# Performance work log

Measured on AMD Instinct MI355X. Metric: run time of the kernel, lower is better.

The kernel has to match this reference:

```python
import jax, jax.numpy as jnp
import numpy as np

EPS = 1e-5

def setup_inputs() -> dict:
    key = jax.random.key(0)
    ks = jax.random.split(key, 8)
    b, c, p, h = 8, 128, 2048, 4
    inp = {
        "input": jax.random.normal(ks[0], (b, c, p), jnp.float32),
        "gamma": jnp.ones((c,), jnp.float32),
        "beta": jnp.zeros((c,), jnp.float32),
        "Wq": jax.random.normal(ks[1], (c * h, c), jnp.float32) * (c ** -0.5),
        "bq": jnp.zeros((c * h,), jnp.float32),
        "Wk": jax.random.normal(ks[2], (c * h, c), jnp.float32) * (c ** -0.5),
        "bk": jnp.zeros((c * h,), jnp.float32),
        "Wv": jax.random.normal(ks[3], (c * h, c), jnp.float32) * (c ** -0.5),
        "bv": jnp.zeros((c * h,), jnp.float32),
        "Wo": jax.random.normal(ks[4], (c, c * h), jnp.float32) * ((c * h) ** -0.5),
        "bo": jnp.zeros((c,), jnp.float32),
    }
    return inp


def reference(input, gamma, beta, Wq, bq, Wk, bk, Wv, bv, Wo, bo):
    b, c, p = input.shape
    h = Wq.shape[0] // c
    # BatchNorm1d (training-mode batch stats): mean/var per channel over (batch, points)
    mean = jnp.mean(input, axis=(0, 2), keepdims=True)          # [1,c,1]
    var = jnp.mean((input - mean) ** 2, axis=(0, 2), keepdims=True)
    x = (input - mean) * jax.lax.rsqrt(var + EPS)
    x = x * gamma[None, :, None] + beta[None, :, None]
    # 1x1 conv projections == channel matmuls; then split c*h -> (c, h)
    q = (jnp.einsum('oc,bcp->bop', Wq, x) + bq[None, :, None]).reshape(b, c, h, p)
    k = (jnp.einsum('oc,bcp->bop', Wk, x) + bk[None, :, None]).reshape(b, c, h, p)
    v = (jnp.einsum('oc,bcp->bop', Wv, x) + bv[None, :, None]).reshape(b, c, h, p)
    # attention over points; scale by c**-0.5
    weight = jnp.einsum('bchi,bchj->bhij', q, k) * (c ** -0.5)   # [b,h,p,p]
    weight = jax.nn.softmax(weight, axis=3)
    att = jnp.einsum('bhij,bchj->bchi', weight, v)               # [b,c,h,p]
    att = att.reshape(b, c * h, p)
    out = jnp.einsum('oc,bcp->bop', Wo, att) + bo[None, :, None]
    return out + input
```

## Files before the change

kernel.cpp:

```cpp
#include <hip/hip_runtime.h>
#include <hip/hip_bf16.h>

#define NB 8
#define NC 128
#define NP 2048
#define NH 4
#define NCH 512

typedef __attribute__((ext_vector_type(8))) short bf16x8;
typedef __attribute__((ext_vector_type(16))) float f32x16;

__device__ __forceinline__ float bf2f(unsigned short u) {
  return __uint_as_float(((unsigned)u) << 16);
}
__device__ __forceinline__ unsigned short f2bf(float f) {
  __hip_bfloat16 h = __float2bfloat16(f);
  return *reinterpret_cast<unsigned short*>(&h);
}
__device__ __forceinline__ unsigned pk2(float lo, float hi) {
  return (unsigned)f2bf(lo) | ((unsigned)f2bf(hi) << 16);
}
__device__ __forceinline__ void gload_lds16(const void* g, void* l) {
  __builtin_amdgcn_global_load_lds(
      (const __attribute__((address_space(1))) void*)g,
      (__attribute__((address_space(3))) void*)l, 16, 0, 0);
}
__device__ __forceinline__ void plswap(unsigned& a, unsigned& b) {
  asm volatile("v_permlane32_swap_b32 %0, %1" : "+v"(a), "+v"(b));
}

__global__ __launch_bounds__(256) void bn_partial(
    const float* __restrict__ in, float* __restrict__ psum,
    float* __restrict__ psum2) {
  int c = blockIdx.x >> 2, qtr = blockIdx.x & 3;
  int t = threadIdx.x;
  float s = 0.f, s2 = 0.f;
  for (int b = 0; b < NB; ++b) {
    const float* ptr = in + ((size_t)b * NC + c) * NP + qtr * 512;
    #pragma unroll
    for (int p = 0; p < 2; ++p) {
      float v = ptr[p * 256 + t];
      s += v; s2 += v * v;
    }
  }
  for (int off = 32; off; off >>= 1) {
    s += __shfl_down(s, off, 64);
    s2 += __shfl_down(s2, off, 64);
  }
  __shared__ float red[8];
  int lane = t & 63, wid = t >> 6;
  if (!lane) { red[wid] = s; red[wid + 4] = s2; }
  __syncthreads();
  if (!t) {
    psum[blockIdx.x] = red[0] + red[1] + red[2] + red[3];
    psum2[blockIdx.x] = red[4] + red[5] + red[6] + red[7];
  }
}

__global__ __launch_bounds__(512, 2) void qkv_proj(
    const float* __restrict__ in, const float* __restrict__ gamma,
    const float* __restrict__ beta, const float* __restrict__ psum,
    const float* __restrict__ psum2, const float* __restrict__ Wq,
    const float* __restrict__ bq, const float* __restrict__ Wk,
    const float* __restrict__ bk, const float* __restrict__ Wv,
    const float* __restrict__ bv, unsigned short* __restrict__ qws,
    unsigned short* __restrict__ kws, unsigned short* __restrict__ vws) {
  __shared__ float sc[128], sh[128], bias[1536];
  __shared__ __align__(16) unsigned short Xt[64][136];
  int t = threadIdx.x;
  int pt = blockIdx.x & 31, b = blockIdx.x >> 5;
  int p0 = pt * 64;
  if (t < 128) {
    float s = psum[t * 4] + psum[t * 4 + 1] + psum[t * 4 + 2] + psum[t * 4 + 3];
    float s2 = psum2[t * 4] + psum2[t * 4 + 1] + psum2[t * 4 + 2] + psum2[t * 4 + 3];
    const float invn = 1.f / (NB * NP);
    float mean = s * invn, var = s2 * invn - mean * mean;
    float scl = gamma[t] * rsqrtf(var + 1e-5f);
    sc[t] = scl; sh[t] = beta[t] - mean * scl;
  }
  bias[t] = bq[t]; bias[512 + t] = bk[t]; bias[1024 + t] = bv[t];
  __syncthreads();
  {
    int p = t & 63, c0 = (t >> 6) * 16;
    const float* src = in + ((size_t)b * NC + c0) * NP + p0 + p;
    #pragma unroll
    for (int cc = 0; cc < 16; ++cc) {
      float v = src[(size_t)cc * NP];
      Xt[p][c0 + cc] = f2bf(v * sc[c0 + cc] + sh[c0 + cc]);
    }
  }
  __syncthreads();
  int w = t >> 6, lane = t & 63, l31 = lane & 31, h5 = lane >> 5;
  #pragma unroll 1
  for (int s = 0; s < 3; ++s) {
    int strip = s * 8 + w;
    int proj = strip >> 3, within = (strip & 7) * 64;
    const float* W = proj == 0 ? Wq : (proj == 1 ? Wk : Wv);
    f32x16 acc[2][2] = {};
    #pragma unroll
    for (int ks = 0; ks < 8; ++ks) {
      bf16x8 af[2], bf[2];
      #pragma unroll
      for (int mt = 0; mt < 2; ++mt) {
        const float* wr = W + (size_t)(within + mt * 32 + l31) * NC + ks * 16 + h5 * 8;
        float4 a = *(const float4*)wr, b4 = *(const float4*)(wr + 4);
        union { bf16x8 v; unsigned u[4]; } uu;
        uu.u[0] = pk2(a.x, a.y); uu.u[1] = pk2(a.z, a.w);
        uu.u[2] = pk2(b4.x, b4.y); uu.u[3] = pk2(b4.z, b4.w);
        af[mt] = uu.v;
      }
      #pragma unroll
      for (int nt = 0; nt < 2; ++nt)
        bf[nt] = *(const bf16x8*)&Xt[nt * 32 + l31][ks * 16 + h5 * 8];
      if (proj < 2) {
        #pragma unroll
        for (int mt = 0; mt < 2; ++mt)
          #pragma unroll
          for (int nt = 0; nt < 2; ++nt)
            acc[mt][nt] = __builtin_amdgcn_mfma_f32_32x32x16_bf16(bf[nt], af[mt], acc[mt][nt], 0, 0, 0);
      } else {
        #pragma unroll
        for (int mt = 0; mt < 2; ++mt)
          #pragma unroll
          for (int nt = 0; nt < 2; ++nt)
            acc[mt][nt] = __builtin_amdgcn_mfma_f32_32x32x16_bf16(af[mt], bf[nt], acc[mt][nt], 0, 0, 0);
      }
    }
    if (proj < 2) {
      unsigned short* dst = proj == 0 ? qws : kws;
      float qs = proj == 0 ? 0.12751743762765621f : 1.0f;
      #pragma unroll
      for (int mt = 0; mt < 2; ++mt) {
        int o = within + mt * 32 + l31;
        float bs = bias[proj * 512 + o];
        unsigned short* drow = dst + ((size_t)(b * 4 + (o & 3)) * NP) * NC + (o >> 2);
        #pragma unroll
        for (int nt = 0; nt < 2; ++nt)
          #pragma unroll
          for (int r = 0; r < 16; ++r) {
            int p = p0 + nt * 32 + (r & 3) + 8 * (r >> 2) + 4 * h5;
            drow[(size_t)p * NC] = f2bf((acc[mt][nt][r] + bs) * qs);
          }
      }
    } else {
      #pragma unroll
      for (int mt = 0; mt < 2; ++mt)
        #pragma unroll
        for (int nt = 0; nt < 2; ++nt)
          #pragma unroll
          for (int r = 0; r < 16; ++r) {
            int oo = within + mt * 32 + (r & 3) + 8 * (r >> 2) + 4 * h5;
            float val = acc[mt][nt][r] + bias[1024 + oo];
            vws[((size_t)(b * NCH + oo)) * NP + p0 + nt * 32 + l31] = f2bf(val);
          }
    }
  }
}

__global__ __launch_bounds__(256, 2) void attn(
    const unsigned short* __restrict__ qT, const unsigned short* __restrict__ kT,
    const unsigned short* __restrict__ vws, unsigned short* __restrict__ attws) {
  __shared__ uint4 Kbuf[2][1024];
  __shared__ uint4 Vbuf[2][1024];
  int tid = threadIdx.x;
  int wl = tid >> 6, lane = tid & 63, l31 = lane & 31, h5 = lane >> 5;
  int bid = blockIdx.x;
  int head = bid & 31, it = bid >> 5;
  int b = head >> 2, hh = head & 3;
  int i0 = it * 128;
  const unsigned short* krow = kT + (size_t)(b * 4 + hh) * NP * NC;
  const unsigned short* vb = vws + (size_t)b * NCH * NP;

  int t4 = tid >> 4;
  int ch = (tid & 15) ^ (t4 & 15);
  size_t vO = ((size_t)((t4 * 2 + (ch >> 3)) * 4 + hh)) * NP + (ch & 7) * 8;

  auto stage = [&](int bi, int j0v) {
    #pragma unroll
    for (int k = 0; k < 4; ++k) {
      gload_lds16(krow + (size_t)(j0v + k * 16 + t4) * NC + (ch << 3),
                  &Kbuf[bi][k * 256 + tid]);
      gload_lds16(vb + vO + (size_t)k * 128 * NP + j0v,
                  &Vbuf[bi][k * 256 + tid]);
    }
  };

  bf16x8 qf[8];
  {
    const unsigned short* qp =
        qT + ((size_t)(b * 4 + hh) * NP + (i0 + wl * 32 + l31)) * NC + h5 * 8;
    #pragma unroll
    for (int ks = 0; ks < 8; ++ks) qf[ks] = *(const bf16x8*)(qp + ks * 16);
  }

  f32x16 oacc[4] = {};
  float lsum = 0.f;

  stage(0, 0);
  __syncthreads();

  int kbase = l31 * 16, ksw = l31 & 15;
  #pragma unroll 1
  for (int tI = 0; tI < 32; ++tI) {
    int cur = tI & 1;
    if (tI < 31) stage(cur ^ 1, (tI + 1) * 64);

    f32x16 sacT0 = {}, sacT1 = {};
    #pragma unroll
    for (int ks = 0; ks < 8; ++ks) {
      int cidx = (ks * 2 + h5) ^ ksw;
      bf16x8 kf0 = *(const bf16x8*)&Kbuf[cur][kbase + cidx];
      bf16x8 kf1 = *(const bf16x8*)&Kbuf[cur][512 + kbase + cidx];
      sacT0 = __builtin_amdgcn_mfma_f32_32x32x16_bf16(kf0, qf[ks], sacT0, 0, 0, 0);
      sacT1 = __builtin_amdgcn_mfma_f32_32x32x16_bf16(kf1, qf[ks], sacT1, 0, 0, 0);
    }
    bf16x8 pfrag[4];
    #pragma unroll
    for (int ntj = 0; ntj < 2; ++ntj) {
      f32x16& sacT = ntj ? sacT1 : sacT0;
      #pragma unroll
      for (int r = 0; r < 16; ++r) {
        sacT[r] = __builtin_amdgcn_exp2f(sacT[r]);
        lsum += sacT[r];
      }
      unsigned wv[8];
      #pragma unroll
      for (int q = 0; q < 8; ++q) wv[q] = pk2(sacT[q * 2], sacT[q * 2 + 1]);
      plswap(wv[0], wv[2]); plswap(wv[1], wv[3]);
      plswap(wv[4], wv[6]); plswap(wv[5], wv[7]);
      union { bf16x8 v; unsigned u[4]; } f0, f1;
      f0.u[0] = wv[0]; f0.u[1] = wv[1]; f0.u[2] = wv[2]; f0.u[3] = wv[3];
      f1.u[0] = wv[4]; f1.u[1] = wv[5]; f1.u[2] = wv[6]; f1.u[3] = wv[7];
      pfrag[ntj * 2] = f0.v; pfrag[ntj * 2 + 1] = f1.v;
    }
    #pragma unroll
    for (int ntc = 0; ntc < 4; ++ntc) {
      int r = ntc * 16 + (l31 >> 1);
      int rb = r * 16, r15 = r & 15, c8 = (l31 & 1) * 8;
      #pragma unroll
      for (int kw = 0; kw < 4; ++kw) {
        bf16x8 vf = *(const bf16x8*)&Vbuf[cur][rb + ((c8 + kw * 2 + h5) ^ r15)];
        oacc[ntc] = __builtin_amdgcn_mfma_f32_32x32x16_bf16(vf, pfrag[kw], oacc[ntc], 0, 0, 0);
      }
    }
    __syncthreads();
  }

  float linv = 1.0f / (lsum + __shfl_xor(lsum, 32, 64));
  int i = i0 + wl * 32 + l31;
  #pragma unroll
  for (int ntc = 0; ntc < 4; ++ntc)
    #pragma unroll
    for (int r = 0; r < 16; ++r) {
      int c = ntc * 32 + (r & 3) + 8 * (r >> 2) + 4 * h5;
      attws[((size_t)(b * NP + i)) * NCH + c * 4 + hh] = f2bf(oacc[ntc][r] * linv);
    }
}

__global__ __launch_bounds__(256, 2) void out_proj(
    const unsigned short* __restrict__ attT, const float* __restrict__ Wo,
    const float* __restrict__ bo, const float* __restrict__ in,
    float* __restrict__ out) {
  __shared__ uint4 Abuf[2][512];
  int t = threadIdx.x;
  int pt = blockIdx.x & 63, b = blockIdx.x >> 6;
  int p0 = pt * 32;
  int w = t >> 6, lane = t & 63, l31 = lane & 31, h5 = lane >> 5;
  const unsigned short* ab = attT + (size_t)b * NP * NCH;
  int row0 = t >> 4, pos = t & 15;
  auto stage = [&](int bi, int k0) {
    #pragma unroll
    for (int q = 0; q < 2; ++q) {
      int row = q * 16 + row0;
      int chq = pos ^ (row & 15);
      gload_lds16(ab + ((size_t)(p0 + row)) * NCH + k0 * 128 + chq * 8,
                  &Abuf[bi][q * 256 + t]);
    }
  };
  f32x16 acc = {};
  stage(0, 0);
  __syncthreads();
  #pragma unroll 1
  for (int k0 = 0; k0 < 4; ++k0) {
    int cur = k0 & 1;
    if (k0 < 3) stage(cur ^ 1, k0 + 1);
    #pragma unroll
    for (int ks = 0; ks < 8; ++ks) {
      const float* wr = Wo + (size_t)(w * 32 + l31) * NCH + k0 * 128 + ks * 16 + h5 * 8;
      float4 a = *(const float4*)wr, b4 = *(const float4*)(wr + 4);
      union { bf16x8 v; unsigned u[4]; } uu;
      uu.u[0] = pk2(a.x, a.y); uu.u[1] = pk2(a.z, a.w);
      uu.u[2] = pk2(b4.x, b4.y); uu.u[3] = pk2(b4.z, b4.w);
      bf16x8 bf = *(const bf16x8*)&Abuf[cur][l31 * 16 + ((ks * 2 + h5) ^ (l31 & 15))];
      acc = __builtin_amdgcn_mfma_f32_32x32x16_bf16(uu.v, bf, acc, 0, 0, 0);
    }
    __syncthreads();
  }
  #pragma unroll
  for (int r = 0; r < 16; ++r) {
    int o = w * 32 + (r & 3) + 8 * (r >> 2) + 4 * h5;
    int p = p0 + l31;
    size_t idx = ((size_t)(b * NC + o)) * NP + p;
    out[idx] = acc[r] + bo[o] + in[idx];
  }
}

extern "C" void kernel_launch(void* const* d_in, const int* in_sizes, int n_in,
                              void* d_out, int out_size, void* d_ws, size_t ws_size,
                              hipStream_t stream) {
  const float* in    = (const float*)d_in[0];
  const float* gamma = (const float*)d_in[1];
  const float* beta  = (const float*)d_in[2];
  const float* Wq = (const float*)d_in[3];
  const float* bq = (const float*)d_in[4];
  const float* Wk = (const float*)d_in[5];
  const float* bk = (const float*)d_in[6];
  const float* Wv = (const float*)d_in[7];
  const float* bv = (const float*)d_in[8];
  const float* Wo = (const float*)d_in[9];
  const float* bo = (const float*)d_in[10];
  float* out = (float*)d_out;

  char* ws = (char*)d_ws;
  float* psum  = (float*)ws;
  float* psum2 = psum + 512;
  const size_t QKV_ELEMS = (size_t)NB * NCH * NP;
  unsigned short* qws   = (unsigned short*)(ws + 8192);
  unsigned short* kws   = qws + QKV_ELEMS;
  unsigned short* vws   = kws + QKV_ELEMS;
  unsigned short* attws = vws + QKV_ELEMS;

  bn_partial<<<dim3(512), dim3(256), 0, stream>>>(in, psum, psum2);
  qkv_proj<<<dim3(256), dim3(512), 0, stream>>>(
      in, gamma, beta, psum, psum2, Wq, bq, Wk, bk, Wv, bv, qws, kws, vws);
  attn<<<dim3(512), dim3(256), 0, stream>>>(qws, kws, vws, attws);
  out_proj<<<dim3(512), dim3(256), 0, stream>>>(attws, Wo, bo, in, out);
}
```

Measured before the change: 224.4 us.

## Interleave Q/K head layout, stage attention output through LDS, pre-permute Wo

Q and K now share one [b, p, 512] layout with the heads interleaved in groups of 8 channels. The attention kernel writes its output through LDS so each head stores contiguous 128-channel rows with 16-byte stores, replacing scattered 2-byte stores at stride 4. A new small kernel converts Wo to bf16 once, permuted to match the new attention layout, so out_proj no longer converts fp32 to bf16 in its inner loop. This adds one extra launch and reuses the q workspace for WoP after attention has finished with it.

```diff
diff --git a/kernel.cpp b/kernel.cpp
--- a/kernel.cpp
+++ b/kernel.cpp
@@ -133,13 +133,15 @@
       for (int mt = 0; mt < 2; ++mt) {
         int o = within + mt * 32 + l31;
         float bs = bias[proj * 512 + o];
-        unsigned short* drow = dst + ((size_t)(b * 4 + (o & 3)) * NP) * NC + (o >> 2);
+        int c = o >> 2;
+        int g = ((c & ~7) << 2) + ((o & 3) << 3) + (c & 7);
+        unsigned short* drow = dst + (size_t)b * NP * NCH + g;
         #pragma unroll
         for (int nt = 0; nt < 2; ++nt)
           #pragma unroll
           for (int r = 0; r < 16; ++r) {
             int p = p0 + nt * 32 + (r & 3) + 8 * (r >> 2) + 4 * h5;
-            drow[(size_t)p * NC] = f2bf((acc[mt][nt][r] + bs) * qs);
+            drow[(size_t)p * NCH] = f2bf((acc[mt][nt][r] + bs) * qs);
           }
       }
     } else {
@@ -168,7 +170,7 @@
   int head = bid & 31, it = bid >> 5;
   int b = head >> 2, hh = head & 3;
   int i0 = it * 128;
-  const unsigned short* krow = kT + (size_t)(b * 4 + hh) * NP * NC;
+  const unsigned short* kb = kT + (size_t)b * NP * NCH;
   const unsigned short* vb = vws + (size_t)b * NCH * NP;
 
   int t4 = tid >> 4;
@@ -178,7 +180,7 @@
   auto stage = [&](int bi, int j0v) {
     #pragma unroll
     for (int k = 0; k < 4; ++k) {
-      gload_lds16(krow + (size_t)(j0v + k * 16 + t4) * NC + (ch << 3),
+      gload_lds16(kb + (size_t)(j0v + k * 16 + t4) * NCH + ch * 32 + hh * 8,
                   &Kbuf[bi][k * 256 + tid]);
       gload_lds16(vb + vO + (size_t)k * 128 * NP + j0v,
                   &Vbuf[bi][k * 256 + tid]);
@@ -188,9 +190,9 @@
   bf16x8 qf[8];
   {
     const unsigned short* qp =
-        qT + ((size_t)(b * 4 + hh) * NP + (i0 + wl * 32 + l31)) * NC + h5 * 8;
-    #pragma unroll
-    for (int ks = 0; ks < 8; ++ks) qf[ks] = *(const bf16x8*)(qp + ks * 16);
+        qT + ((size_t)b * NP + (i0 + wl * 32 + l31)) * NCH + h5 * 32 + hh * 8;
+    #pragma unroll
+    for (int ks = 0; ks < 8; ++ks) qf[ks] = *(const bf16x8*)(qp + ks * 64);
   }
 
   f32x16 oacc[4] = {};
@@ -247,18 +249,45 @@
   }
 
   float linv = 1.0f / (lsum + __shfl_xor(lsum, 32, 64));
-  int i = i0 + wl * 32 + l31;
+  unsigned short* TB = (unsigned short*)Kbuf;
+  int iL = wl * 32 + l31;
+  int isw = iL & 7;
   #pragma unroll
   for (int ntc = 0; ntc < 4; ++ntc)
     #pragma unroll
     for (int r = 0; r < 16; ++r) {
       int c = ntc * 32 + (r & 3) + 8 * (r >> 2) + 4 * h5;
-      attws[((size_t)(b * NP + i)) * NCH + c * 4 + hh] = f2bf(oacc[ntc][r] * linv);
-    }
+      TB[iL * 128 + (((c >> 3) ^ isw) << 3) + (c & 7)] = f2bf(oacc[ntc][r] * linv);
+    }
+  __syncthreads();
+  {
+    int i2 = tid >> 1, half = tid & 1;
+    unsigned short* gp = attws + ((size_t)b * NP + i0 + i2) * NCH + hh * 128 + half * 64;
+    const unsigned short* rp = TB + i2 * 128;
+    int sw2 = i2 & 7;
+    #pragma unroll
+    for (int q = 0; q < 8; ++q) {
+      int ck = half * 8 + q;
+      uint4 v = *(const uint4*)(rp + ((ck ^ sw2) << 3));
+      *(uint4*)(gp + q * 8) = v;
+    }
+  }
+}
+
+__global__ __launch_bounds__(256) void wo_perm(
+    const float* __restrict__ Wo, unsigned short* __restrict__ WoP) {
+  int idx = (blockIdx.x * 256 + threadIdx.x) * 4;
+  int o = idx >> 9, g0 = idx & 511;
+  int hh = g0 >> 7;
+  const float* src = Wo + (size_t)o * NCH + (g0 & 127) * 4 + hh;
+  union { unsigned short u[4]; uint2 v; } tmp;
+  #pragma unroll
+  for (int e = 0; e < 4; ++e) tmp.u[e] = f2bf(src[e * 4]);
+  *(uint2*)(WoP + idx) = tmp.v;
 }
 
 __global__ __launch_bounds__(256, 2) void out_proj(
-    const unsigned short* __restrict__ attT, const float* __restrict__ Wo,
+    const unsigned short* __restrict__ attT, const unsigned short* __restrict__ WoP,
     const float* __restrict__ bo, const float* __restrict__ in,
     float* __restrict__ out) {
   __shared__ uint4 Abuf[2][512];
@@ -286,13 +315,9 @@
     if (k0 < 3) stage(cur ^ 1, k0 + 1);
     #pragma unroll
     for (int ks = 0; ks < 8; ++ks) {
-      const float* wr = Wo + (size_t)(w * 32 + l31) * NCH + k0 * 128 + ks * 16 + h5 * 8;
-      float4 a = *(const float4*)wr, b4 = *(const float4*)(wr + 4);
-      union { bf16x8 v; unsigned u[4]; } uu;
-      uu.u[0] = pk2(a.x, a.y); uu.u[1] = pk2(a.z, a.w);
-      uu.u[2] = pk2(b4.x, b4.y); uu.u[3] = pk2(b4.z, b4.w);
+      bf16x8 af = *(const bf16x8*)(WoP + (size_t)(w * 32 + l31) * NCH + k0 * 128 + ks * 16 + h5 * 8);
       bf16x8 bf = *(const bf16x8*)&Abuf[cur][l31 * 16 + ((ks * 2 + h5) ^ (l31 & 15))];
-      acc = __builtin_amdgcn_mfma_f32_32x32x16_bf16(uu.v, bf, acc, 0, 0, 0);
+      acc = __builtin_amdgcn_mfma_f32_32x32x16_bf16(af, bf, acc, 0, 0, 0);
     }
     __syncthreads();
   }
@@ -329,10 +354,12 @@
   unsigned short* kws   = qws + QKV_ELEMS;
   unsigned short* vws   = kws + QKV_ELEMS;
   unsigned short* attws = vws + QKV_ELEMS;
+  unsigned short* WoP   = qws;
 
   bn_partial<<<dim3(512), dim3(256), 0, stream>>>(in, psum, psum2);
   qkv_proj<<<dim3(256), dim3(512), 0, stream>>>(
       in, gamma, beta, psum, psum2, Wq, bq, Wk, bk, Wv, bv, qws, kws, vws);
   attn<<<dim3(512), dim3(256), 0, stream>>>(qws, kws, vws, attws);
-  out_proj<<<dim3(512), dim3(256), 0, stream>>>(attws, Wo, bo, in, out);
-}
+  wo_perm<<<dim3(64), dim3(256), 0, stream>>>(Wo, WoP);
+  out_proj<<<dim3(512), dim3(256), 0, stream>>>(attws, WoP, bo, in, out);
+}
```

After: 210.4 us. -6.3%, faster.
